# Kernel optimization log

Hardware: AMD Instinct MI355X
Metric: run time of the kernel (lower is better)

Reference implementation:

```python
import jax, jax.numpy as jnp
import numpy as np

N = 16384
D = 512
K = 1024          # fixed num_clusters (torch code uses randint(2, N//2))
NUM_ITERS = 10    # kmeans Lloyd iterations
NUM_CLUSTER_ITERS = 1
TEMPERATURE = 0.1
CONCENTRATION = 0.1
EPS = 1e-6


def setup_inputs() -> dict:
    key = jax.random.key(0)
    feats = jax.random.normal(key, (N, D), dtype=jnp.float32)
    return {"feats": feats}


def _assign(feats, centroids, x_sq):
    c_sq = jnp.sum(centroids * centroids, axis=-1)            # [K]
    d = x_sq[:, None] - 2.0 * (feats @ centroids.T) + c_sq[None, :]
    return jnp.argmin(d, axis=-1)                             # [N] int32


def _kmeans(feats, num_clusters, num_iters):
    x_sq = jnp.sum(feats * feats, axis=-1)                    # [N]
    init_centroids = feats[:num_clusters]                     # deterministic init

    def body(_, centroids):
        clusters = _assign(feats, centroids, x_sq)
        sums = jax.ops.segment_sum(feats, clusters, num_segments=num_clusters)
        counts = jax.ops.segment_sum(jnp.ones((feats.shape[0],), feats.dtype),
                                     clusters, num_segments=num_clusters)
        new_c = sums / jnp.maximum(counts, 1.0)[:, None]
        # keep old centroid for empty clusters
        return jnp.where(counts[:, None] > 0, new_c, centroids)

    centroids = jax.lax.fori_loop(0, num_iters, body, init_centroids)
    clusters = _assign(feats, centroids, x_sq)
    counts = jax.ops.segment_sum(jnp.ones((feats.shape[0],), feats.dtype),
                                 clusters, num_segments=num_clusters)
    return clusters, centroids, counts


def reference(feats):
    clusters, centroids, _ = _kmeans(feats, K, NUM_ITERS)
    # per-point squared residuals gathered by cluster id, scatter-added to [K, D]
    resid2 = (feats - centroids[clusters]) ** 2               # [N, D]
    dists = jax.ops.segment_sum(resid2, clusters, num_segments=K)  # [K, D]
    # entropy loss branch (concentration phi)
    p = jnp.exp(-dists / CONCENTRATION)
    Q = p / jnp.sum(p)
    entropy = jnp.mean(Q * jnp.log(Q + EPS)) / NUM_CLUSTER_ITERS
    # nll branch (temperature t)
    p2 = jnp.exp(-dists / TEMPERATURE)
    nll = -jnp.mean(jnp.log(p2 + EPS))
    return entropy + nll
```

## Files before the change

### kernel.cpp

```cpp
#include <hip/hip_runtime.h>
#include <math.h>

#define N 16384
#define D 512
#define K 1024
#define NUM_ITERS 10
#define TEMPERATURE 0.1f
#define CONCENTRATION 0.1f
#define EPS 1e-6f

typedef unsigned short ushort_t;
typedef unsigned int uint_t;
typedef unsigned long long u64;
typedef __attribute__((ext_vector_type(4))) float floatx4;
typedef __attribute__((ext_vector_type(8))) short shortx8;

__device__ inline ushort_t f2h(float f) {
    _Float16 h = (_Float16)f;
    return *(ushort_t*)&h;
}

__device__ inline unsigned ford(float f) {
    unsigned b = __float_as_uint(f);
    return (b & 0x80000000u) ? ~b : (b | 0x80000000u);
}

__device__ inline void f4add(float4& a, const float4& b) {
    a.x += b.x; a.y += b.y; a.z += b.z; a.w += b.w;
}

__device__ inline void gld16(const void* g, void* l) {
    __builtin_amdgcn_global_load_lds(
        (const __attribute__((address_space(1))) void*)(uintptr_t)(g),
        (__attribute__((address_space(3))) void*)(uintptr_t)(l), 16, 0, 0);
}

#define WAITVM(n_lit) asm volatile("s_waitcnt vmcnt(" #n_lit ")" ::: "memory")

#define SPLIT_BLOCKS (N * D / 4 / 256)
__global__ void split_kernel(const float* __restrict__ x, ushort_t* __restrict__ hi,
                             u64* __restrict__ best2, float* __restrict__ cent,
                             double* __restrict__ scal, float* __restrict__ csq) {
    const int bid = blockIdx.x;
    const int tid = threadIdx.x;
    if (bid < SPLIT_BLOCKS) {
        int i = bid * 256 + tid;
        float4 v = ((const float4*)x)[i];
        ushort4 hv = {f2h(v.x), f2h(v.y), f2h(v.z), f2h(v.w)};
        ((ushort4*)hi)[i] = hv;
        if (i < 2 * N) best2[i] = ~0ull;
        if (i < K * D / 4) ((float4*)cent)[i] = v;
        if (i == 0) { scal[0] = 0.0; scal[1] = 0.0; scal[2] = 0.0; *(int*)&scal[3] = 0; }
    } else {
        int row = (bid - SPLIT_BLOCKS) * 4 + (tid >> 6);
        int lane = tid & 63;
        if (row >= K) return;
        const float* r = x + (size_t)row * D;
        float s = 0.f;
        for (int i = lane; i < D; i += 64) { float v = r[i]; s += v * v; }
        for (int off = 32; off > 0; off >>= 1) s += __shfl_down(s, off, 64);
        if (lane == 0) csq[row] = s;
    }
}

__global__ __launch_bounds__(512, 4) void assign_mfma3(
    const ushort_t* __restrict__ Ah, const ushort_t* __restrict__ Bh,
    const float* __restrict__ csq, u64* __restrict__ best)
{
    __shared__ __align__(16) ushort_t sA[3 * 8192];
    __shared__ __align__(16) ushort_t sB[3 * 4096];

    const int tid = threadIdx.x;
    const int lane = tid & 63;
    const int wave = tid >> 6;
    const int wr = wave >> 1, wc = wave & 1;
    const int quad = lane >> 4, l16 = lane & 15;

    const int bid = (int)blockIdx.x;
    const int xid = bid & 7;
    const int s = bid >> 3;
    const int brow = (xid << 3) + (s >> 3);
    const int bcol = s & 7;
    const int row0 = brow * 256, col0 = bcol * 128;

    floatx4 acc[4][4];
#pragma unroll
    for (int a = 0; a < 4; ++a)
#pragma unroll
        for (int b = 0; b < 4; ++b) acc[a][b] = (floatx4){0.f, 0.f, 0.f, 0.f};

    const int swz = (quad ^ (l16 & 3) ^ ((l16 >> 2) & 3)) * 8;
    const int aoff = (wr * 64 + l16) * 32 + swz;
    const int boff = (wc * 64 + l16) * 32 + swz;

    auto stage = [&](int t2) {
        const int r = t2 % 3;
        ushort_t* dA = sA + r * 8192;
        ushort_t* dB = sB + r * 4096;
        const int d0 = t2 * 32;
#pragma unroll
        for (int ii = 0; ii < 2; ++ii) {
            const int idx = ii * 512 + tid;
            const int row = idx >> 2;
            const int kb = (idx & 3) ^ (row & 3) ^ ((row >> 2) & 3);
            gld16(Ah + (size_t)(row0 + row) * D + d0 + kb * 8, dA + idx * 8);
        }
        {
            const int idx = tid;
            const int row = idx >> 2;
            const int kb = (idx & 3) ^ (row & 3) ^ ((row >> 2) & 3);
            gld16(Bh + (size_t)(col0 + row) * D + d0 + kb * 8, dB + idx * 8);
        }
    };

    stage(0); stage(1);
    WAITVM(3);
    __builtin_amdgcn_s_barrier();
    __builtin_amdgcn_sched_barrier(0);

#pragma unroll
    for (int t = 0; t < 16; ++t) {
        if (t + 2 < 16) stage(t + 2);
        const ushort_t* Ar = sA + (t % 3) * 8192;
        const ushort_t* Br = sB + (t % 3) * 4096;
        shortx8 fa[4], fb[4];
#pragma unroll
        for (int j = 0; j < 4; ++j) fb[j] = *(const shortx8*)&Br[boff + j * 512];
#pragma unroll
        for (int i = 0; i < 4; ++i) fa[i] = *(const shortx8*)&Ar[aoff + i * 512];
        __builtin_amdgcn_s_setprio(1);
#pragma unroll
        for (int i = 0; i < 4; ++i)
#pragma unroll
            for (int j = 0; j < 4; ++j)
                acc[i][j] = __builtin_amdgcn_mfma_f32_16x16x32_f16(
                    fa[i], fb[j], acc[i][j], 0, 0, 0);
        __builtin_amdgcn_s_setprio(0);
        if (t < 15) {
            asm volatile("s_waitcnt lgkmcnt(0)" ::: "memory");
            if (t < 14) { WAITVM(3); } else { WAITVM(0); }
            __builtin_amdgcn_s_barrier();
            __builtin_amdgcn_sched_barrier(0);
        }
    }

    float csqv[4];
#pragma unroll
    for (int j = 0; j < 4; ++j) csqv[j] = csq[col0 + wc * 64 + j * 16 + l16];

    const int k0 = col0 + wc * 64 + l16;
#pragma unroll
    for (int i = 0; i < 4; ++i) {
#pragma unroll
        for (int r = 0; r < 4; ++r) {
            float bv = csqv[0] - 2.0f * acc[i][0][r];
            int bk = k0;
#pragma unroll
            for (int j = 1; j < 4; ++j) {
                float v = csqv[j] - 2.0f * acc[i][j][r];
                int kk = k0 + j * 16;
                if (v < bv || (v == bv && kk < bk)) { bv = v; bk = kk; }
            }
#pragma unroll
            for (int m = 1; m < 16; m <<= 1) {
                float ov = __shfl_xor(bv, m, 64);
                int ok = __shfl_xor(bk, m, 64);
                if (ov < bv || (ov == bv && ok < bk)) { bv = ov; bk = ok; }
            }
            if (l16 == 0) {
                int p = row0 + wr * 64 + i * 16 + quad * 4 + r;
                u64 pk = ((u64)ford(bv) << 32) | (unsigned)bk;
                atomicMin(&best[p], pk);
            }
        }
    }
}

#define CU_WAVES 8
#define CHUNKS (N / 128)
#define ROUNDS 4
#define WIN (CHUNKS / ROUNDS)
#define CPW (WIN / CU_WAVES)

__global__ __launch_bounds__(512) void cluster_update(
    const float* __restrict__ feats, const u64* __restrict__ best,
    u64* __restrict__ best_other,
    float* __restrict__ cent, ushort_t* __restrict__ Bh,
    float* __restrict__ csq)
{
    __shared__ int list[CU_WAVES][CPW * 128];
    __shared__ int lcnt[CU_WAVES];
    __shared__ float4 part[CU_WAVES][64][2];
    __shared__ int pcnt_s[CU_WAVES];

    const int tid = threadIdx.x;
    const int lane = tid & 63;
    const int wave = tid >> 6;
    const int k = (int)blockIdx.x;

    float4 a0 = {0.f, 0.f, 0.f, 0.f}, a1 = {0.f, 0.f, 0.f, 0.f};
    int cnttot = 0;

    for (int round = 0; round < ROUNDS; ++round) {
        int cw = 0;
#pragma unroll
        for (int cc = 0; cc < CPW; ++cc) {
            int chunk = round * WIN + wave * CPW + cc;
            ulonglong2 v = ((const ulonglong2*)best)[chunk * 64 + lane];
            int id0 = (int)(uint_t)v.x;
            int id1 = (int)(uint_t)v.y;
            int p0 = chunk * 128 + 2 * lane;
            u64 m0 = __ballot(id0 == k);
            u64 m1 = __ballot(id1 == k);
            int c0 = __popcll(m0);
            u64 lanem = (1ull << lane) - 1ull;
            if (id0 == k) list[wave][cw + __popcll(m0 & lanem)] = p0;
            if (id1 == k) list[wave][cw + c0 + __popcll(m1 & lanem)] = p0 + 1;
            cw += c0 + __popcll(m1);
        }
        if (lane == 0) lcnt[wave] = cw;
        cnttot += cw;
        __syncthreads();

        int off[CU_WAVES]; int T = 0;
#pragma unroll
        for (int j = 0; j < CU_WAVES; ++j) { off[j] = T; T += lcnt[j]; }

        for (int g0 = wave; g0 < T; g0 += CU_WAVES * 4) {
            int nb = 0; int pidx[4];
#pragma unroll
            for (int b = 0; b < 4; ++b) {
                int g = g0 + CU_WAVES * b;
                if (g < T) {
                    int j = 0;
#pragma unroll
                    for (int jj = 1; jj < CU_WAVES; ++jj) if (g >= off[jj]) j = jj;
                    pidx[nb++] = list[j][g - off[j]];
                }
            }
            float4 x[4][2];
#pragma unroll
            for (int b = 0; b < 4; ++b) if (b < nb) {
                const float4* r = (const float4*)(feats + (size_t)pidx[b] * D) + lane * 2;
                x[b][0] = r[0]; x[b][1] = r[1];
            }
#pragma unroll
            for (int b = 0; b < 4; ++b) if (b < nb) {
                f4add(a0, x[b][0]); f4add(a1, x[b][1]);
            }
        }
        __syncthreads();
    }

    part[wave][lane][0] = a0; part[wave][lane][1] = a1;
    if (lane == 0) pcnt_s[wave] = cnttot;
    __syncthreads();

    if (wave == 0) {
        float4 s0 = part[0][lane][0], s1 = part[0][lane][1];
        int c = pcnt_s[0];
#pragma unroll
        for (int w = 1; w < CU_WAVES; ++w) {
            f4add(s0, part[w][lane][0]); f4add(s1, part[w][lane][1]);
            c += pcnt_s[w];
        }

        float4* crow = (float4*)(cent + (size_t)k * D) + lane * 2;
        float4 c0, c1;
        if (c > 0) {
            float cf = (float)c;
            c0 = (float4){s0.x / cf, s0.y / cf, s0.z / cf, s0.w / cf};
            c1 = (float4){s1.x / cf, s1.y / cf, s1.z / cf, s1.w / cf};
        } else {
            c0 = crow[0]; c1 = crow[1];
        }
        crow[0] = c0; crow[1] = c1;

        ushort4 hv;
        hv.x = f2h(c0.x); hv.y = f2h(c0.y); hv.z = f2h(c0.z); hv.w = f2h(c0.w);
        ((ushort4*)(Bh + (size_t)k * D))[lane * 2] = hv;
        hv.x = f2h(c1.x); hv.y = f2h(c1.y); hv.z = f2h(c1.z); hv.w = f2h(c1.w);
        ((ushort4*)(Bh + (size_t)k * D))[lane * 2 + 1] = hv;

        float s = c0.x * c0.x + c0.y * c0.y + c0.z * c0.z + c0.w * c0.w
                + c1.x * c1.x + c1.y * c1.y + c1.z * c1.z + c1.w * c1.w;
        for (int o = 32; o > 0; o >>= 1) s += __shfl_xor(s, o, 64);
        if (lane == 0) csq[k] = s;
    }

    if (tid < 16) best_other[k * 16 + tid] = ~0ull;
}

__global__ __launch_bounds__(512) void dist_gather(
    const float* __restrict__ feats, const float* __restrict__ cent,
    const u64* __restrict__ best, float* __restrict__ dists)
{
    __shared__ int list[CU_WAVES][CPW * 128];
    __shared__ int lcnt[CU_WAVES];
    __shared__ float4 part[CU_WAVES][64][2];

    const int tid = threadIdx.x;
    const int lane = tid & 63;
    const int wave = tid >> 6;
    const int k = (int)blockIdx.x;

    const float4* crow = (const float4*)(cent + (size_t)k * D) + lane * 2;
    const float4 c0 = crow[0], c1 = crow[1];

    float4 a0 = {0.f, 0.f, 0.f, 0.f}, a1 = {0.f, 0.f, 0.f, 0.f};

    for (int round = 0; round < ROUNDS; ++round) {
        int cw = 0;
#pragma unroll
        for (int cc = 0; cc < CPW; ++cc) {
            int chunk = round * WIN + wave * CPW + cc;
            ulonglong2 v = ((const ulonglong2*)best)[chunk * 64 + lane];
            int id0 = (int)(uint_t)v.x;
            int id1 = (int)(uint_t)v.y;
            int p0 = chunk * 128 + 2 * lane;
            u64 m0 = __ballot(id0 == k);
            u64 m1 = __ballot(id1 == k);
            int cc0 = __popcll(m0);
            u64 lanem = (1ull << lane) - 1ull;
            if (id0 == k) list[wave][cw + __popcll(m0 & lanem)] = p0;
            if (id1 == k) list[wave][cw + cc0 + __popcll(m1 & lanem)] = p0 + 1;
            cw += cc0 + __popcll(m1);
        }
        if (lane == 0) lcnt[wave] = cw;
        __syncthreads();

        int off[CU_WAVES]; int T = 0;
#pragma unroll
        for (int j = 0; j < CU_WAVES; ++j) { off[j] = T; T += lcnt[j]; }

        for (int g0 = wave; g0 < T; g0 += CU_WAVES * 4) {
            int nb = 0; int pidx[4];
#pragma unroll
            for (int b = 0; b < 4; ++b) {
                int g = g0 + CU_WAVES * b;
                if (g < T) {
                    int j = 0;
#pragma unroll
                    for (int jj = 1; jj < CU_WAVES; ++jj) if (g >= off[jj]) j = jj;
                    pidx[nb++] = list[j][g - off[j]];
                }
            }
            float4 x[4][2];
#pragma unroll
            for (int b = 0; b < 4; ++b) if (b < nb) {
                const float4* r = (const float4*)(feats + (size_t)pidx[b] * D) + lane * 2;
                x[b][0] = r[0]; x[b][1] = r[1];
            }
#pragma unroll
            for (int b = 0; b < 4; ++b) if (b < nb) {
                float r;
                r = x[b][0].x - c0.x; a0.x += r * r;  r = x[b][0].y - c0.y; a0.y += r * r;
                r = x[b][0].z - c0.z; a0.z += r * r;  r = x[b][0].w - c0.w; a0.w += r * r;
                r = x[b][1].x - c1.x; a1.x += r * r;  r = x[b][1].y - c1.y; a1.y += r * r;
                r = x[b][1].z - c1.z; a1.z += r * r;  r = x[b][1].w - c1.w; a1.w += r * r;
            }
        }
        __syncthreads();
    }

    part[wave][lane][0] = a0; part[wave][lane][1] = a1;
    __syncthreads();
    if (wave == 0) {
        float4 s0 = part[0][lane][0], s1 = part[0][lane][1];
#pragma unroll
        for (int w = 1; w < CU_WAVES; ++w) { f4add(s0, part[w][lane][0]); f4add(s1, part[w][lane][1]); }
        float4* drow = (float4*)(dists + (size_t)k * D) + lane * 2;
        drow[0] = s0; drow[1] = s1;
    }
}

__global__ void loss_fused(const float* __restrict__ dists, double* __restrict__ scal,
                           float* __restrict__ out) {
    const int tid = threadIdx.x;
    int* cnt = (int*)&scal[3];
    __shared__ float red[4];
    __shared__ double Sbc;

    float v = 0.f;
    for (int idx = blockIdx.x * 256 + tid; idx < K * D; idx += 256 * 256)
        v += expf(-(dists[idx] / CONCENTRATION));
    for (int off = 32; off > 0; off >>= 1) v += __shfl_down(v, off, 64);
    if ((tid & 63) == 0) red[tid >> 6] = v;
    __syncthreads();
    if (tid == 0) {
        atomicAdd(&scal[0], (double)(red[0] + red[1] + red[2] + red[3]));
        __threadfence();
        atomicAdd(cnt, 1);
        while (atomicAdd(cnt, 0) < 256) __builtin_amdgcn_s_sleep(1);
        Sbc = atomicAdd(&scal[0], 0.0);
    }
    __syncthreads();
    const float S = (float)Sbc;

    float e = 0.f, nl = 0.f;
    for (int idx = blockIdx.x * 256 + tid; idx < K * D; idx += 256 * 256) {
        float dv = dists[idx];
        float p = expf(-(dv / CONCENTRATION));
        float qq = p / S;
        e += qq * logf(qq + EPS);
        float p2 = expf(-(dv / TEMPERATURE));
        nl += logf(p2 + EPS);
    }
    __shared__ float rede[4];
    __shared__ float redn[4];
    for (int off = 32; off > 0; off >>= 1) { e += __shfl_down(e, off, 64); nl += __shfl_down(nl, off, 64); }
    if ((tid & 63) == 0) { rede[tid >> 6] = e; redn[tid >> 6] = nl; }
    __syncthreads();
    if (tid == 0) {
        atomicAdd(&scal[1], (double)(rede[0] + rede[1] + rede[2] + rede[3]));
        atomicAdd(&scal[2], (double)(redn[0] + redn[1] + redn[2] + redn[3]));
        __threadfence();
        int t = atomicAdd(cnt, 1);
        if (t == 511) {
            double e_s = atomicAdd(&scal[1], 0.0);
            double n_s = atomicAdd(&scal[2], 0.0);
            double kd = (double)(K * D);
            double entropy = e_s / kd;
            double nll = -(n_s / kd);
            out[0] = (float)(entropy + nll);
        }
    }
}

extern "C" void kernel_launch(void* const* d_in, const int* in_sizes, int n_in,
                              void* d_out, int out_size, void* d_ws, size_t ws_size,
                              hipStream_t stream) {
    const float* feats = (const float*)d_in[0];
    float* out = (float*)d_out;

    ushort_t* Ah = (ushort_t*)d_ws;
    ushort_t* Bh = Ah + (size_t)N * D;
    float* centroids = (float*)(Bh + (size_t)K * D);
    float* dists     = centroids + (size_t)K * D;
    float* csq       = dists + (size_t)K * D;
    u64*   best0     = (u64*)(csq + K);
    u64*   best1     = best0 + N;
    double* scal     = (double*)(best1 + N);

    split_kernel<<<SPLIT_BLOCKS + K / 4, 256, 0, stream>>>(feats, Ah, best0, centroids,
                                                           scal, csq);

    for (int it = 0; it < NUM_ITERS; ++it) {
        u64* cur = (it & 1) ? best1 : best0;
        u64* oth = (it & 1) ? best0 : best1;
        const ushort_t* bh = (it == 0) ? Ah : Bh;
        assign_mfma3<<<(N / 256) * (K / 128), 512, 0, stream>>>(Ah, bh, csq, cur);
        cluster_update<<<K, 512, 0, stream>>>(feats, cur, oth, centroids, Bh, csq);
    }
    u64* fin = (NUM_ITERS & 1) ? best1 : best0;
    assign_mfma3<<<(N / 256) * (K / 128), 512, 0, stream>>>(Ah, Bh, csq, fin);

    dist_gather<<<K, 512, 0, stream>>>(feats, centroids, fin, dists);

    loss_fused<<<256, 256, 0, stream>>>(dists, scal, out);
}
```

Before: 672.8 us.

## Load A fragments directly to registers and deepen B LDS pipeline

The assign GEMM kernel stops staging the A (points) tile through shared memory. Each wave now loads its A fragments straight from global memory into a double-buffered register array two steps ahead. The B (centroid) tile stays in LDS with a 5-slot ring prefetched four steps ahead, and the vmcnt waits are retuned to match. This removes LDS traffic and capacity for A and raises prefetch depth, at the cost of uncoalesced-ish 16-byte global loads per lane and more registers.

```diff
diff --git a/kernel.cpp b/kernel.cpp
--- a/kernel.cpp
+++ b/kernel.cpp
@@ -63,12 +63,11 @@
     }
 }
 
-__global__ __launch_bounds__(512, 4) void assign_mfma3(
+__global__ __launch_bounds__(512, 4) void assign_mfma4(
     const ushort_t* __restrict__ Ah, const ushort_t* __restrict__ Bh,
     const float* __restrict__ csq, u64* __restrict__ best)
 {
-    __shared__ __align__(16) ushort_t sA[3 * 8192];
-    __shared__ __align__(16) ushort_t sB[3 * 4096];
+    __shared__ __align__(16) ushort_t sB[5 * 4096];
 
     const int tid = threadIdx.x;
     const int lane = tid & 63;
@@ -90,55 +89,54 @@
         for (int b = 0; b < 4; ++b) acc[a][b] = (floatx4){0.f, 0.f, 0.f, 0.f};
 
     const int swz = (quad ^ (l16 & 3) ^ ((l16 >> 2) & 3)) * 8;
-    const int aoff = (wr * 64 + l16) * 32 + swz;
     const int boff = (wc * 64 + l16) * 32 + swz;
 
-    auto stage = [&](int t2) {
-        const int r = t2 % 3;
-        ushort_t* dA = sA + r * 8192;
-        ushort_t* dB = sB + r * 4096;
-        const int d0 = t2 * 32;
-#pragma unroll
-        for (int ii = 0; ii < 2; ++ii) {
-            const int idx = ii * 512 + tid;
-            const int row = idx >> 2;
-            const int kb = (idx & 3) ^ (row & 3) ^ ((row >> 2) & 3);
-            gld16(Ah + (size_t)(row0 + row) * D + d0 + kb * 8, dA + idx * 8);
-        }
-        {
-            const int idx = tid;
-            const int row = idx >> 2;
-            const int kb = (idx & 3) ^ (row & 3) ^ ((row >> 2) & 3);
-            gld16(Bh + (size_t)(col0 + row) * D + d0 + kb * 8, dB + idx * 8);
-        }
+    const ushort_t* Abase = Ah + (size_t)(row0 + wr * 64 + l16) * D + quad * 8;
+
+    shortx8 fabuf[2][4];
+
+    auto loadA = [&](int t2) {
+#pragma unroll
+        for (int i = 0; i < 4; ++i)
+            fabuf[t2 & 1][i] = *(const shortx8*)(Abase + (size_t)(i * 16) * D + t2 * 32);
     };
 
-    stage(0); stage(1);
+    auto stageB = [&](int t2) {
+        const int slot = t2 % 5;
+        const int row = tid >> 2;
+        const int kb = (tid & 3) ^ (row & 3) ^ ((row >> 2) & 3);
+        gld16(Bh + (size_t)(col0 + row) * D + t2 * 32 + kb * 8,
+              sB + slot * 4096 + tid * 8);
+    };
+
+    loadA(0); loadA(1);
+    stageB(0); stageB(1); stageB(2); stageB(3);
     WAITVM(3);
     __builtin_amdgcn_s_barrier();
     __builtin_amdgcn_sched_barrier(0);
 
 #pragma unroll
     for (int t = 0; t < 16; ++t) {
-        if (t + 2 < 16) stage(t + 2);
-        const ushort_t* Ar = sA + (t % 3) * 8192;
-        const ushort_t* Br = sB + (t % 3) * 4096;
-        shortx8 fa[4], fb[4];
+        const ushort_t* Br = sB + (t % 5) * 4096;
+        shortx8 fb[4];
 #pragma unroll
         for (int j = 0; j < 4; ++j) fb[j] = *(const shortx8*)&Br[boff + j * 512];
-#pragma unroll
-        for (int i = 0; i < 4; ++i) fa[i] = *(const shortx8*)&Ar[aoff + i * 512];
         __builtin_amdgcn_s_setprio(1);
 #pragma unroll
         for (int i = 0; i < 4; ++i)
 #pragma unroll
             for (int j = 0; j < 4; ++j)
                 acc[i][j] = __builtin_amdgcn_mfma_f32_16x16x32_f16(
-                    fa[i], fb[j], acc[i][j], 0, 0, 0);
+                    fabuf[t & 1][i], fb[j], acc[i][j], 0, 0, 0);
         __builtin_amdgcn_s_setprio(0);
+        if (t + 2 < 16) loadA(t + 2);
+        if (t + 4 < 16) stageB(t + 4);
         if (t < 15) {
             asm volatile("s_waitcnt lgkmcnt(0)" ::: "memory");
-            if (t < 14) { WAITVM(3); } else { WAITVM(0); }
+            if (t <= 11)      { WAITVM(6); }
+            else if (t == 12) { WAITVM(5); }
+            else if (t == 13) { WAITVM(4); }
+            else              { WAITVM(0); }
             __builtin_amdgcn_s_barrier();
             __builtin_amdgcn_sched_barrier(0);
         }
@@ -449,11 +447,11 @@
         u64* cur = (it & 1) ? best1 : best0;
         u64* oth = (it & 1) ? best0 : best1;
         const ushort_t* bh = (it == 0) ? Ah : Bh;
-        assign_mfma3<<<(N / 256) * (K / 128), 512, 0, stream>>>(Ah, bh, csq, cur);
+        assign_mfma4<<<(N / 256) * (K / 128), 512, 0, stream>>>(Ah, bh, csq, cur);
         cluster_update<<<K, 512, 0, stream>>>(feats, cur, oth, centroids, Bh, csq);
     }
     u64* fin = (NUM_ITERS & 1) ? best1 : best0;
-    assign_mfma3<<<(N / 256) * (K / 128), 512, 0, stream>>>(Ah, Bh, csq, fin);
+    assign_mfma4<<<(N / 256) * (K / 128), 512, 0, stream>>>(Ah, Bh, csq, fin);
 
     dist_gather<<<K, 512, 0, stream>>>(feats, centroids, fin, dists);
 
```

New measurement: 825.9 us. 1.23x slower.
